# Kernel tuning notes

Measured on AMD Instinct MI355X. Metric: run time of the kernel, lower is better.

The kernel has to match this reference:

```python
import jax, jax.numpy as jnp
import numpy as np


def fps(xyz, npoint):
    # farthest point sampling, starts at index 0 (matches pointnet2 CUDA kernel)
    B, N, _ = xyz.shape
    def step(carry, _):
        min_d, last = carry
        last_xyz = jnp.take_along_axis(xyz, last[:, None, None], axis=1)  # [B,1,3]
        d = jnp.sum((xyz - last_xyz) ** 2, axis=-1)                        # [B,N]
        min_d = jnp.minimum(min_d, d)
        nxt = jnp.argmax(min_d, axis=1).astype(jnp.int32)
        return (min_d, nxt), last
    init = (jnp.full((B, N), 1e10, xyz.dtype), jnp.zeros((B,), jnp.int32))
    _, idx = jax.lax.scan(step, init, None, length=npoint)
    return jnp.transpose(idx)  # [B, npoint]


def ball_query(xyz, new_xyz, radius, nsample):
    # first nsample points within radius; pad with first hit (0 if none) -- CUDA semantics
    N = xyz.shape[1]
    d2 = jnp.sum((new_xyz[:, :, None, :] - xyz[:, None, :, :]) ** 2, axis=-1)  # [B,S,N]
    cand = jnp.where(d2 < radius * radius, jnp.arange(N, dtype=jnp.int32)[None, None, :], N)
    srt = jnp.sort(cand, axis=-1)[..., :nsample]
    first = srt[..., :1]
    first = jnp.where(first == N, 0, first)
    return jnp.where(srt == N, first, srt)  # [B,S,K]


def gather_nbrs(x, idx):
    # x [B,N,C], idx [B,S,K] -> [B,S,K,C]
    B, S, K = idx.shape
    flat = jnp.take_along_axis(x, idx.reshape(B, S * K, 1), axis=1)
    return flat.reshape(B, S, K, x.shape[-1])


def shared_mlp(x, layers):
    # 1x1 conv (+ folded eval-mode BN) + ReLU per layer
    for w, b in layers:
        x = jax.nn.relu(jnp.einsum('bskc,oc->bsko', x, w) + b)
    return x


def sa_module(xyz, feat, npoint, radius, nsample, layers):
    idx = fps(xyz, npoint)
    new_xyz = jnp.take_along_axis(xyz, idx[:, :, None], axis=1)  # [B,S,3]
    gidx = ball_query(xyz, new_xyz, radius, nsample)
    grouped = gather_nbrs(xyz, gidx) - new_xyz[:, :, None, :]    # centered local xyz
    if feat is not None:
        grouped = jnp.concatenate([grouped, gather_nbrs(feat, gidx)], axis=-1)
    x = shared_mlp(grouped, layers)
    return new_xyz, jnp.max(x, axis=2)  # max-pool over neighbors -> [B,S,Cout]


def sa_module_all(xyz, feat, layers):
    # GroupAll: concat raw (uncentered) xyz with features, one group of all points
    x = jnp.concatenate([xyz, feat], axis=-1)[:, None]  # [B,1,N,3+C]
    x = shared_mlp(x, layers)
    return jnp.max(x, axis=2)[:, 0]  # [B,Cout]


def _forward(data, ws):
    B, T, N, _ = data.shape
    xyz = data.reshape(B * T, N, 3)
    xyz, feat = sa_module(xyz, None, 256, 0.2, 32, ws[0])
    xyz, feat = sa_module(xyz, feat, 128, 0.4, 32, ws[1])
    out = sa_module_all(xyz, feat, ws[2])
    return out.reshape(B, T, -1)


DIMS = [(3, 64), (64, 64), (64, 128), (131, 128), (128, 128), (128, 256), (259, 256), (256, 512), (512, 1024)]
NAMES = ['1_0', '1_1', '1_2', '2_0', '2_1', '2_2', '3_0', '3_1', '3_2']


def setup_inputs() -> dict:
    key = jax.random.key(0)
    keys = jax.random.split(key, 1 + 2 * len(DIMS))
    inp = {'data': jax.random.normal(keys[0], (4, 8, 4096, 3), jnp.float32)}
    for i, ((cin, cout), nm) in enumerate(zip(DIMS, NAMES)):
        inp['w' + nm] = jax.random.normal(keys[1 + 2 * i], (cout, cin), jnp.float32) / np.sqrt(cin).astype(np.float32)
        inp['b' + nm] = jax.random.normal(keys[2 + 2 * i], (cout,), jnp.float32) * 0.02
    return inp


def reference(data, w1_0, b1_0, w1_1, b1_1, w1_2, b1_2,
              w2_0, b2_0, w2_1, b2_1, w2_2, b2_2,
              w3_0, b3_0, w3_1, b3_1, w3_2, b3_2):
    ws = [[(w1_0, b1_0), (w1_1, b1_1), (w1_2, b1_2)],
          [(w2_0, b2_0), (w2_1, b2_1), (w2_2, b2_2)],
          [(w3_0, b3_0), (w3_1, b3_1), (w3_2, b3_2)]]
    return _forward(data, ws)
```

## Files before the change

kernel.cpp:

```cpp
#include <hip/hip_runtime.h>
#include <hip/hip_bf16.h>
#include <cstdint>
#include <cstddef>

#define BT 32
#define N1 4096
#define S1 256
#define S2 128
#define KNB 32

typedef __attribute__((ext_vector_type(8))) short short8;
typedef __attribute__((ext_vector_type(4))) float f32x4;

__device__ __forceinline__ float sqdist(float ax, float ay, float az,
                                        float bx, float by, float bz) {
    float dx = __fsub_rn(ax, bx), dy = __fsub_rn(ay, by), dz = __fsub_rn(az, bz);
    return __fadd_rn(__fadd_rn(__fmul_rn(dx, dx), __fmul_rn(dy, dy)), __fmul_rn(dz, dz));
}

__device__ __forceinline__ unsigned short f2bf(float f) {
    unsigned u = __float_as_uint(f);
    return (unsigned short)((u + 0x7FFFu + ((u >> 16) & 1u)) >> 16);
}
__device__ __forceinline__ float bf2f(unsigned short h) {
    return __uint_as_float(((unsigned)h) << 16);
}

__device__ __forceinline__ unsigned long long packvi(float v, int idx) {
    return ((unsigned long long)__float_as_uint(v) << 32) | (unsigned)(~idx);
}

template <int CTRL>
__device__ __forceinline__ unsigned long long dppmax(unsigned long long v) {
    int lo = (int)(unsigned)(v & 0xFFFFFFFFull);
    int hi = (int)(unsigned)(v >> 32);
    int lo2 = __builtin_amdgcn_update_dpp(0, lo, CTRL, 0xF, 0xF, false);
    int hi2 = __builtin_amdgcn_update_dpp(0, hi, CTRL, 0xF, 0xF, false);
    unsigned long long o = ((unsigned long long)(unsigned)hi2 << 32) | (unsigned)lo2;
    return o > v ? o : v;
}
#define ROR1 0x121
#define ROR2 0x122
#define ROR4 0x124
#define ROR8 0x128

__global__ __launch_bounds__(256) void fps1_wconv_kernel(
    const float* __restrict__ xyz, float* __restrict__ nxz,
    const float* __restrict__ w11, const float* __restrict__ w12,
    const float* __restrict__ w20, const float* __restrict__ w21,
    const float* __restrict__ w22, const float* __restrict__ w30,
    const float* __restrict__ w31, const float* __restrict__ w32,
    unsigned short* __restrict__ wb) {
    if (blockIdx.x < 32) {
        const int b = blockIdx.x, tid = threadIdx.x;
        const int lane = tid & 63, wv = tid >> 6;
        const float* X = xyz + (size_t)b * (N1 * 3);
        __shared__ float4 s4[N1];
        __shared__ unsigned long long slots[2][16];
        __shared__ float hist[S1 * 3];
        float px[16], py[16], pz[16], md[16];
        int bidx[16];
#pragma unroll
        for (int j = 0; j < 16; ++j) {
            int i = tid + 256 * j;
            float x = X[i * 3 + 0], y = X[i * 3 + 1], z = X[i * 3 + 2];
            s4[i] = make_float4(x, y, z, 0.f);
            px[j] = x; py[j] = y; pz[j] = z;
            md[j] = 1e10f;
            bidx[j] = i;
        }
        if (tid == 0) { hist[0] = X[0]; hist[1] = X[1]; hist[2] = X[2]; }
        __syncthreads();
        float4 c0 = s4[0];
        float lx = c0.x, ly = c0.y, lz = c0.z;
        for (int t = 1; t < S1; ++t) {
            float bv = -1.0f; int bi = 0;
#pragma unroll
            for (int j = 0; j < 16; ++j) {
                float d = sqdist(px[j], py[j], pz[j], lx, ly, lz);
                float m = fminf(md[j], d);
                md[j] = m;
                if (m > bv) { bv = m; bi = bidx[j]; }
            }
            unsigned long long best = packvi(bv, bi);
            best = dppmax<ROR1>(best);
            best = dppmax<ROR2>(best);
            best = dppmax<ROR4>(best);
            best = dppmax<ROR8>(best);
            if ((lane & 15) == 0) slots[t & 1][wv * 4 + (lane >> 4)] = best;
            __syncthreads();
            unsigned long long w = slots[t & 1][lane & 15];
            w = dppmax<ROR1>(w);
            w = dppmax<ROR2>(w);
            w = dppmax<ROR4>(w);
            w = dppmax<ROR8>(w);
            int vi = (int)(~(unsigned)w);
            float4 c = s4[vi];
            lx = c.x; ly = c.y; lz = c.z;
            if (tid == 0) { hist[t * 3 + 0] = lx; hist[t * 3 + 1] = ly; hist[t * 3 + 2] = lz; }
        }
        __syncthreads();
        for (int u = tid; u < S1 * 3; u += 256) nxz[(size_t)b * S1 * 3 + u] = hist[u];
    } else {
        int u = (blockIdx.x - 32) * 256 + threadIdx.x;
        if (u >= 823296) return;
        const float* src; int base, Kp, Ko; int perm = 0;
        if      (u < 4096)   { src = w11; base = 0;      Kp = 64;  Ko = 64;  }
        else if (u < 12288)  { src = w12; base = 4096;   Kp = 64;  Ko = 64;  }
        else if (u < 36864)  { src = w20; base = 12288;  Kp = 192; Ko = 131; perm = 128; }
        else if (u < 53248)  { src = w21; base = 36864;  Kp = 128; Ko = 128; }
        else if (u < 86016)  { src = w22; base = 53248;  Kp = 128; Ko = 128; }
        else if (u < 167936) { src = w30; base = 86016;  Kp = 320; Ko = 259; perm = 256; }
        else if (u < 299008) { src = w31; base = 167936; Kp = 256; Ko = 256; }
        else                 { src = w32; base = 299008; Kp = 512; Ko = 512; }
        int local = u - base;
        int n = local / Kp, k = local - n * Kp;
        float v;
        if (perm) {
            int ksrc = (k < perm) ? (k + 3) : ((k < perm + 3) ? (k - perm) : -1);
            v = (ksrc >= 0) ? src[(size_t)n * Ko + ksrc] : 0.f;
        } else {
            v = (k < Ko) ? src[(size_t)n * Ko + k] : 0.f;
        }
        wb[u] = f2bf(v);
    }
}

__global__ __launch_bounds__(256) void ballq1_kernel(const float* __restrict__ xyz,
                                                     const float* __restrict__ nxz,
                                                     int* __restrict__ gidx) {
    const int wid = (blockIdx.x * 256 + threadIdx.x) >> 6;
    const int lane = threadIdx.x & 63;
    const int b = wid >> 8;
    const float* X = xyz + (size_t)b * (N1 * 3);
    const float* C = nxz + (size_t)wid * 3;
    const float cx = C[0], cy = C[1], cz = C[2];
    const float r2 = (float)(0.2 * 0.2);
    int* G = gidx + (size_t)wid * KNB;
    int cnt = 0, first = 0;
    bool found = false;
    for (int j0 = 0; j0 < N1 && cnt < KNB; j0 += 64) {
        int j = j0 + lane;
        float d2 = sqdist(cx, cy, cz, X[j * 3 + 0], X[j * 3 + 1], X[j * 3 + 2]);
        bool hit = d2 < r2;
        unsigned long long mask = __ballot(hit);
        if (!found && mask) { first = j0 + __builtin_ctzll(mask); found = true; }
        if (hit) {
            int pos = cnt + __popcll(mask & ((1ull << lane) - 1ull));
            if (pos < KNB) G[pos] = j;
        }
        cnt += __popcll(mask);
    }
    if (cnt < KNB) {
        int pad = found ? first : 0;
        if (lane >= cnt && lane < KNB) G[lane] = pad;
    }
}

__global__ __launch_bounds__(256) void m1_fps2_kernel(
    const float* __restrict__ xyz, const float* __restrict__ nxz,
    const int* __restrict__ g1,
    const float* __restrict__ w10, const float* __restrict__ b10,
    const unsigned short* __restrict__ w11b, const float* __restrict__ b11,
    const unsigned short* __restrict__ w12b, const float* __restrict__ b12,
    unsigned short* __restrict__ f1,
    float* __restrict__ nxz2) {
    if (blockIdx.x < 32) {
        if (threadIdx.x >= 64) return;
        const int b = blockIdx.x, lane = threadIdx.x;
        const float* X = nxz + (size_t)b * (S1 * 3);
        __shared__ float4 s4f[S1];
        float px[4], py[4], pz[4], md[4];
        int bidx[4];
#pragma unroll
        for (int j = 0; j < 4; ++j) {
            int i = lane + 64 * j;
            float x = X[i * 3 + 0], y = X[i * 3 + 1], z = X[i * 3 + 2];
            s4f[i] = make_float4(x, y, z, 0.f);
            px[j] = x; py[j] = y; pz[j] = z;
            md[j] = 1e10f;
            bidx[j] = i;
        }
        if (lane == 0) {
            nxz2[(size_t)b * S2 * 3 + 0] = X[0];
            nxz2[(size_t)b * S2 * 3 + 1] = X[1];
            nxz2[(size_t)b * S2 * 3 + 2] = X[2];
        }
        float4 cc = s4f[0];
        float lx = cc.x, ly = cc.y, lz = cc.z;
        for (int t = 1; t < S2; ++t) {
            float bv = -1.0f; int bi = 0;
#pragma unroll
            for (int j = 0; j < 4; ++j) {
                float d = sqdist(px[j], py[j], pz[j], lx, ly, lz);
                float m = fminf(md[j], d);
                md[j] = m;
                if (m > bv) { bv = m; bi = bidx[j]; }
            }
            unsigned long long best = packvi(bv, bi);
            best = dppmax<ROR1>(best);
            best = dppmax<ROR2>(best);
            best = dppmax<ROR4>(best);
            best = dppmax<ROR8>(best);
            { unsigned long long o = __shfl_xor(best, 16); best = o > best ? o : best; }
            { unsigned long long o = __shfl_xor(best, 32); best = o > best ? o : best; }
            int vi = (int)(~(unsigned)best);
            float4 c = s4f[vi];
            lx = c.x; ly = c.y; lz = c.z;
            if (lane == 0) {
                float* dst = nxz2 + ((size_t)b * S2 + t) * 3;
                dst[0] = lx; dst[1] = ly; dst[2] = lz;
            }
        }
        return;
    }
    constexpr int AP = 72;
    __shared__ __align__(16) unsigned short As[128 * AP];
    __shared__ __align__(16) unsigned short Hs[128 * AP];
    __shared__ __align__(16) unsigned short Bs[192 * AP];
    __shared__ float sxyz[128 * 3];
    const int t = threadIdx.x;
    const int lane = t & 63, w = t >> 6;
    const int r16 = lane & 15, q = lane >> 4;
    const int m0 = (blockIdx.x - 32) * 128;

    if (t < 128) {
        int row = m0 + t, bs = row >> 5, b = bs >> 8, j = g1[row];
        const float* P = xyz + ((size_t)b * N1 + j) * 3;
        const float* Cc = nxz + (size_t)bs * 3;
        sxyz[t * 3 + 0] = P[0] - Cc[0];
        sxyz[t * 3 + 1] = P[1] - Cc[1];
        sxyz[t * 3 + 2] = P[2] - Cc[2];
    }
    for (int c = t; c < 192 * 8; c += 256) {
        int row = c >> 3, ch = c & 7;
        const unsigned short* src = (row < 64) ? &w11b[row * 64 + ch * 8]
                                               : &w12b[(row - 64) * 64 + ch * 8];
        *(short8*)&Bs[row * AP + ch * 8] = *(const short8*)src;
    }
    __syncthreads();
    {
        const int r = t >> 1, half = (t & 1) * 32;
        const float x = sxyz[r * 3 + 0], y = sxyz[r * 3 + 1], z = sxyz[r * 3 + 2];
        unsigned short tmp[32];
#pragma unroll
        for (int o = 0; o < 32; ++o) {
            int oo = half + o;
            float acc = b10[oo];
            acc = fmaf(x, w10[oo * 3 + 0], acc);
            acc = fmaf(y, w10[oo * 3 + 1], acc);
            acc = fmaf(z, w10[oo * 3 + 2], acc);
            tmp[o] = f2bf(fmaxf(acc, 0.f));
        }
#pragma unroll
        for (int c2 = 0; c2 < 4; ++c2)
            *(short8*)&As[r * AP + half + c2 * 8] = *(short8*)&tmp[c2 * 8];
    }
    __syncthreads();
    {
        f32x4 acc[2][4];
#pragma unroll
        for (int i = 0; i < 2; ++i)
#pragma unroll
            for (int j = 0; j < 4; ++j) acc[i][j] = (f32x4){0.f, 0.f, 0.f, 0.f};
#pragma unroll
        for (int kk = 0; kk < 64; kk += 32) {
            short8 a0 = *(const short8*)&As[(w * 32 + r16) * AP + kk + q * 8];
            short8 a1 = *(const short8*)&As[(w * 32 + 16 + r16) * AP + kk + q * 8];
#pragma unroll
            for (int j = 0; j < 4; ++j) {
                short8 bf = *(const short8*)&Bs[(j * 16 + r16) * AP + kk + q * 8];
                acc[0][j] = __builtin_amdgcn_mfma_f32_16x16x32_bf16(a0, bf, acc[0][j], 0, 0, 0);
                acc[1][j] = __builtin_amdgcn_mfma_f32_16x16x32_bf16(a1, bf, acc[1][j], 0, 0, 0);
            }
        }
#pragma unroll
        for (int i = 0; i < 2; ++i)
#pragma unroll
            for (int j = 0; j < 4; ++j) {
                int col = j * 16 + r16;
                float bv = b11[col];
#pragma unroll
                for (int r = 0; r < 4; ++r) {
                    int row = w * 32 + i * 16 + q * 4 + r;
                    Hs[row * AP + col] = f2bf(fmaxf(acc[i][j][r] + bv, 0.f));
                }
            }
    }
    __syncthreads();
    {
        f32x4 acc[2][8];
#pragma unroll
        for (int i = 0; i < 2; ++i)
#pragma unroll
            for (int j = 0; j < 8; ++j) acc[i][j] = (f32x4){0.f, 0.f, 0.f, 0.f};
#pragma unroll
        for (int kk = 0; kk < 64; kk += 32) {
            short8 a0 = *(const short8*)&Hs[(w * 32 + r16) * AP + kk + q * 8];
            short8 a1 = *(const short8*)&Hs[(w * 32 + 16 + r16) * AP + kk + q * 8];
#pragma unroll
            for (int j = 0; j < 8; ++j) {
                short8 bf = *(const short8*)&Bs[(64 + j * 16 + r16) * AP + kk + q * 8];
                acc[0][j] = __builtin_amdgcn_mfma_f32_16x16x32_bf16(a0, bf, acc[0][j], 0, 0, 0);
                acc[1][j] = __builtin_amdgcn_mfma_f32_16x16x32_bf16(a1, bf, acc[1][j], 0, 0, 0);
            }
        }
#pragma unroll
        for (int j = 0; j < 8; ++j) {
            int col = j * 16 + r16;
            float bv = b12[col];
            float mv = 0.f;
#pragma unroll
            for (int i = 0; i < 2; ++i)
#pragma unroll
                for (int r = 0; r < 4; ++r)
                    mv = fmaxf(mv, acc[i][j][r] + bv);
            mv = fmaxf(mv, __shfl_xor(mv, 16));
            mv = fmaxf(mv, __shfl_xor(mv, 32));
            if (q == 0)
                f1[(size_t)((m0 >> 5) + w) * 128 + col] = f2bf(mv);
        }
    }
}

__global__ __launch_bounds__(256) void ballq2_kernel(const float* __restrict__ xyz1,
                                                     const float* __restrict__ nxz2,
                                                     int* __restrict__ gidx) {
    const int wid = (blockIdx.x * 256 + threadIdx.x) >> 6;
    const int lane = threadIdx.x & 63;
    const int b = wid >> 7;
    const float* X = xyz1 + (size_t)b * (S1 * 3);
    const float* C = nxz2 + (size_t)wid * 3;
    const float cx = C[0], cy = C[1], cz = C[2];
    const float r2 = (float)(0.4 * 0.4);
    int* G = gidx + (size_t)wid * KNB;
    int cnt = 0, first = 0;
    bool found = false;
    for (int j0 = 0; j0 < S1 && cnt < KNB; j0 += 64) {
        int j = j0 + lane;
        float d2 = sqdist(cx, cy, cz, X[j * 3 + 0], X[j * 3 + 1], X[j * 3 + 2]);
        bool hit = d2 < r2;
        unsigned long long mask = __ballot(hit);
        if (!found && mask) { first = j0 + __builtin_ctzll(mask); found = true; }
        if (hit) {
            int pos = cnt + __popcll(mask & ((1ull << lane) - 1ull));
            if (pos < KNB) G[pos] = j;
        }
        cnt += __popcll(mask);
    }
    if (cnt < KNB) {
        int pad = found ? first : 0;
        if (lane >= cnt && lane < KNB) G[lane] = pad;
    }
}

__global__ __launch_bounds__(256) void m2_kernel(
    const float* __restrict__ xyz1, const float* __restrict__ nxz2,
    const int* __restrict__ g2, const unsigned short* __restrict__ f1,
    const unsigned short* __restrict__ w20p, const float* __restrict__ b20,
    const unsigned short* __restrict__ w21b, const float* __restrict__ b21,
    const unsigned short* __restrict__ w22b, const float* __restrict__ b22,
    unsigned short* __restrict__ f2) {
    constexpr int AP = 72, HP = 136;
    __shared__ __align__(16) unsigned short smem[36864];
    unsigned short* R1 = smem;
    unsigned short* R2 = smem + 18432;
    unsigned short* As = R1;
    unsigned short* Bs = R1 + 9216;
    unsigned short* W21 = R1;
    unsigned short* H1 = R2;
    unsigned short* H2 = R1;
    unsigned short* Bs2 = R2;
    __shared__ int ribase[128];
    __shared__ unsigned short sxb[128 * 3];
    const int t = threadIdx.x;
    const int lane = t & 63, w = t >> 6;
    const int r16 = lane & 15, q = lane >> 4;
    const int m0 = blockIdx.x * 128;

    if (t < 128) {
        int row = m0 + t, bs = row >> 5, b = bs >> 7, j = g2[row];
        ribase[t] = (b * 256 + j) * 128;
        const float* P = xyz1 + ((size_t)b * S1 + j) * 3;
        const float* Cc = nxz2 + (size_t)bs * 3;
        sxb[t * 3 + 0] = f2bf(P[0] - Cc[0]);
        sxb[t * 3 + 1] = f2bf(P[1] - Cc[1]);
        sxb[t * 3 + 2] = f2bf(P[2] - Cc[2]);
    }
    __syncthreads();

    f32x4 acc[2][8];
#pragma unroll
    for (int i = 0; i < 2; ++i)
#pragma unroll
        for (int j = 0; j < 8; ++j) acc[i][j] = (f32x4){0.f, 0.f, 0.f, 0.f};
    for (int kt = 0; kt < 3; ++kt) {
        const int k0 = kt * 64;
        if (kt < 2) {
            for (int c = t; c < 128 * 8; c += 256) {
                int row = c >> 3, ch = c & 7;
                *(short8*)&As[row * AP + ch * 8] =
                    *(const short8*)&f1[(size_t)ribase[row] + k0 + ch * 8];
            }
        } else {
            for (int c = t; c < 128 * 8; c += 256) {
                int row = c >> 3, ch = c & 7;
                short8 v = (short8){0, 0, 0, 0, 0, 0, 0, 0};
                if (ch == 0) {
                    v[0] = (short)sxb[row * 3 + 0];
                    v[1] = (short)sxb[row * 3 + 1];
                    v[2] = (short)sxb[row * 3 + 2];
                }
                *(short8*)&As[row * AP + ch * 8] = v;
            }
        }
        for (int c = t; c < 128 * 8; c += 256) {
            int row = c >> 3, ch = c & 7;
            *(short8*)&Bs[row * AP + ch * 8] =
                *(const short8*)&w20p[(size_t)row * 192 + k0 + ch * 8];
        }
        __syncthreads();
#pragma unroll
        for (int kk = 0; kk < 64; kk += 32) {
            short8 a0 = *(const short8*)&As[(w * 32 + r16) * AP + kk + q * 8];
            short8 a1 = *(const short8*)&As[(w * 32 + 16 + r16) * AP + kk + q * 8];
#pragma unroll
            for (int j = 0; j < 8; ++j) {
                short8 bf = *(const short8*)&Bs[(j * 16 + r16) * AP + kk + q * 8];
                acc[0][j] = __builtin_amdgcn_mfma_f32_16x16x32_bf16(a0, bf, acc[0][j], 0, 0, 0);
                acc[1][j] = __builtin_amdgcn_mfma_f32_16x16x32_bf16(a1, bf, acc[1][j], 0, 0, 0);
            }
        }
        __syncthreads();
    }
#pragma unroll
    for (int i = 0; i < 2; ++i)
#pragma unroll
        for (int j = 0; j < 8; ++j) {
            int col = j * 16 + r16;
            float bv = b20[col];
#pragma unroll
            for (int r = 0; r < 4; ++r) {
                int row = w * 32 + i * 16 + q * 4 + r;
                H1[row * HP + col] = f2bf(fmaxf(acc[i][j][r] + bv, 0.f));
            }
        }
    __syncthreads();
    for (int c = t; c < 128 * 16; c += 256) {
        int row = c >> 4, ch = c & 15;
        *(short8*)&W21[row * HP + ch * 8] =
            *(const short8*)&w21b[(size_t)row * 128 + ch * 8];
    }
    __syncthreads();
#pragma unroll
    for (int i = 0; i < 2; ++i)
#pragma unroll
        for (int j = 0; j < 8; ++j) acc[i][j] = (f32x4){0.f, 0.f, 0.f, 0.f};
#pragma unroll
    for (int kk = 0; kk < 128; kk += 32) {
        short8 a0 = *(const short8*)&H1[(w * 32 + r16) * HP + kk + q * 8];
        short8 a1 = *(const short8*)&H1[(w * 32 + 16 + r16) * HP + kk + q * 8];
#pragma unroll
        for (int j = 0; j < 8; ++j) {
            short8 bf = *(const short8*)&W21[(j * 16 + r16) * HP + kk + q * 8];
            acc[0][j] = __builtin_amdgcn_mfma_f32_16x16x32_bf16(a0, bf, acc[0][j], 0, 0, 0);
            acc[1][j] = __builtin_amdgcn_mfma_f32_16x16x32_bf16(a1, bf, acc[1][j], 0, 0, 0);
        }
    }
    __syncthreads();
#pragma unroll
    for (int i = 0; i < 2; ++i)
#pragma unroll
        for (int j = 0; j < 8; ++j) {
            int col = j * 16 + r16;
            float bv = b21[col];
#pragma unroll
            for (int r = 0; r < 4; ++r) {
                int row = w * 32 + i * 16 + q * 4 + r;
                H2[row * HP + col] = f2bf(fmaxf(acc[i][j][r] + bv, 0.f));
            }
        }
    __syncthreads();

    f32x4 acc2[2][16];
#pragma unroll
    for (int i = 0; i < 2; ++i)
#pragma unroll
        for (int j = 0; j < 16; ++j) acc2[i][j] = (f32x4){0.f, 0.f, 0.f, 0.f};
    for (int kt = 0; kt < 2; ++kt) {
        const int k0 = kt * 64;
        for (int c = t; c < 256 * 8; c += 256) {
            int row = c >> 3, ch = c & 7;
            *(short8*)&Bs2[row * AP + ch * 8] =
                *(const short8*)&w22b[(size_t)row * 128 + k0 + ch * 8];
        }
        __syncthreads();
#pragma unroll
        for (int kk = 0; kk < 64; kk += 32) {
            short8 a0 = *(const short8*)&H2[(w * 32 + r16) * HP + k0 + kk + q * 8];
            short8 a1 = *(const short8*)&H2[(w * 32 + 16 + r16) * HP + k0 + kk + q * 8];
#pragma unroll
            for (int j = 0; j < 16; ++j) {
                short8 bf = *(const short8*)&Bs2[(j * 16 + r16) * AP + kk + q * 8];
                acc2[0][j] = __builtin_amdgcn_mfma_f32_16x16x32_bf16(a0, bf, acc2[0][j], 0, 0, 0);
                acc2[1][j] = __builtin_amdgcn_mfma_f32_16x16x32_bf16(a1, bf, acc2[1][j], 0, 0, 0);
            }
        }
        __syncthreads();
    }
#pragma unroll
    for (int j = 0; j < 16; ++j) {
        int col = j * 16 + r16;
        float bv = b22[col];
        float mv = 0.f;
#pragma unroll
        for (int i = 0; i < 2; ++i)
#pragma unroll
            for (int r = 0; r < 4; ++r)
                mv = fmaxf(mv, acc2[i][j][r] + bv);
        mv = fmaxf(mv, __shfl_xor(mv, 16));
        mv = fmaxf(mv, __shfl_xor(mv, 32));
        if (q == 0)
            f2[(size_t)((m0 >> 5) + w) * 256 + col] = f2bf(mv);
    }
}

__global__ __launch_bounds__(256) void l30_kernel(
    const float* __restrict__ nxz2, const unsigned short* __restrict__ f2,
    const unsigned short* __restrict__ w30p, const float* __restrict__ bias,
    unsigned short* __restrict__ C) {
    constexpr int AP = 72;
    __shared__ __align__(16) unsigned short As[128 * AP];
    __shared__ __align__(16) unsigned short Bs[128 * AP];
    const int t = threadIdx.x;
    const int lane = t & 63, w = t >> 6;
    const int r16 = lane & 15, q = lane >> 4;
    const int m0 = blockIdx.x * 128;
    const int n0 = blockIdx.y * 128;

    f32x4 acc[2][8];
#pragma unroll
    for (int i = 0; i < 2; ++i)
#pragma unroll
        for (int j = 0; j < 8; ++j) acc[i][j] = (f32x4){0.f, 0.f, 0.f, 0.f};

    for (int kt = 0; kt < 5; ++kt) {
        const int k0 = kt * 64;
        if (kt < 4) {
            for (int c = t; c < 128 * 8; c += 256) {
                int row = c >> 3, ch = c & 7;
                *(short8*)&As[row * AP + ch * 8] =
                    *(const short8*)&f2[(size_t)(m0 + row) * 256 + k0 + ch * 8];
            }
        } else {
            for (int c = t; c < 128 * 8; c += 256) {
                int row = c >> 3, ch = c & 7;
                short8 v = (short8){0, 0, 0, 0, 0, 0, 0, 0};
                if (ch == 0) {
                    const float* P = nxz2 + (size_t)(m0 + row) * 3;
                    v[0] = (short)f2bf(P[0]);
                    v[1] = (short)f2bf(P[1]);
                    v[2] = (short)f2bf(P[2]);
                }
                *(short8*)&As[row * AP + ch * 8] = v;
            }
        }
        for (int c = t; c < 128 * 8; c += 256) {
            int row = c >> 3, ch = c & 7;
            *(short8*)&Bs[row * AP + ch * 8] =
                *(const short8*)&w30p[(size_t)(n0 + row) * 320 + k0 + ch * 8];
        }
        __syncthreads();
#pragma unroll
        for (int kk = 0; kk < 64; kk += 32) {
            short8 a0 = *(const short8*)&As[(w * 32 + r16) * AP + kk + q * 8];
            short8 a1 = *(const short8*)&As[(w * 32 + 16 + r16) * AP + kk + q * 8];
#pragma unroll
            for (int j = 0; j < 8; ++j) {
                short8 bf = *(const short8*)&Bs[(j * 16 + r16) * AP + kk + q * 8];
                acc[0][j] = __builtin_amdgcn_mfma_f32_16x16x32_bf16(a0, bf, acc[0][j], 0, 0, 0);
                acc[1][j] = __builtin_amdgcn_mfma_f32_16x16x32_bf16(a1, bf, acc[1][j], 0, 0, 0);
            }
        }
        __syncthreads();
    }
#pragma unroll
    for (int i = 0; i < 2; ++i)
#pragma unroll
        for (int j = 0; j < 8; ++j) {
            int col = n0 + j * 16 + r16;
            float bv = bias[col];
#pragma unroll
            for (int r = 0; r < 4; ++r) {
                int row = m0 + w * 32 + i * 16 + q * 4 + r;
                C[(size_t)row * 256 + col] = f2bf(fmaxf(acc[i][j][r] + bv, 0.f));
            }
        }
}

template <int BM_>
__global__ __launch_bounds__(256) void mfma_gemm(const unsigned short* __restrict__ X,
                                                 const unsigned short* __restrict__ W,
                                                 const float* __restrict__ bias,
                                                 unsigned short* __restrict__ C,
                                                 int M, int N, int K) {
    constexpr int BK = 64, AP = BK + 8;
    constexpr int RW = BM_ / 64;
    constexpr int WR = BM_ / 4;
    __shared__ __align__(16) unsigned short As[BM_ * AP];
    __shared__ __align__(16) unsigned short Bs[128 * AP];
    const int t = threadIdx.x;
    const int lane = t & 63, w = t >> 6;
    const int m0 = blockIdx.x * BM_;
    const int n0 = blockIdx.y * 128;
    const int r16 = lane & 15, q = lane >> 4;

    f32x4 acc[RW][8];
#pragma unroll
    for (int i = 0; i < RW; ++i)
#pragma unroll
        for (int j = 0; j < 8; ++j) acc[i][j] = (f32x4){0.f, 0.f, 0.f, 0.f};

    for (int k0 = 0; k0 < K; k0 += BK) {
        for (int c = t; c < BM_ * 8; c += 256) {
            int row = c >> 3, ch = c & 7;
            *(short8*)&As[row * AP + ch * 8] =
                *(const short8*)&X[(size_t)(m0 + row) * K + k0 + ch * 8];
        }
        for (int c = t; c < 128 * 8; c += 256) {
            int row = c >> 3, ch = c & 7;
            *(short8*)&Bs[row * AP + ch * 8] =
                *(const short8*)&W[(size_t)(n0 + row) * K + k0 + ch * 8];
        }
        __syncthreads();
#pragma unroll
        for (int kk = 0; kk < BK; kk += 32) {
            short8 a[RW];
#pragma unroll
            for (int i = 0; i < RW; ++i)
                a[i] = *(const short8*)&As[(w * WR + i * 16 + r16) * AP + kk + q * 8];
#pragma unroll
            for (int j = 0; j < 8; ++j) {
                short8 bf = *(const short8*)&Bs[(j * 16 + r16) * AP + kk + q * 8];
#pragma unroll
                for (int i = 0; i < RW; ++i)
                    acc[i][j] = __builtin_amdgcn_mfma_f32_16x16x32_bf16(a[i], bf, acc[i][j], 0, 0, 0);
            }
        }
        __syncthreads();
    }
#pragma unroll
    for (int i = 0; i < RW; ++i)
#pragma unroll
        for (int j = 0; j < 8; ++j) {
            int col = n0 + j * 16 + r16;
            float bv = bias[col];
#pragma unroll
            for (int r = 0; r < 4; ++r) {
                int row = m0 + w * WR + i * 16 + q * 4 + r;
                C[(size_t)row * N + col] = f2bf(fmaxf(acc[i][j][r] + bv, 0.f));
            }
        }
}

__global__ __launch_bounds__(256) void gemm_pool128(const unsigned short* __restrict__ X,
                                                    const unsigned short* __restrict__ W,
                                                    const float* __restrict__ bias,
                                                    float* __restrict__ out) {
    constexpr int BK = 64, AP = BK + 8, K = 512;
    __shared__ __align__(16) unsigned short As[128 * AP];
    __shared__ __align__(16) unsigned short Bs[128 * AP];
    __shared__ float pool[4][128];
    const int t = threadIdx.x;
    const int lane = t & 63, w = t >> 6;
    const int m0 = blockIdx.x * 128;
    const int n0 = blockIdx.y * 128;
    const int r16 = lane & 15, q = lane >> 4;

    f32x4 acc[2][8];
#pragma unroll
    for (int i = 0; i < 2; ++i)
#pragma unroll
        for (int j = 0; j < 8; ++j) acc[i][j] = (f32x4){0.f, 0.f, 0.f, 0.f};

    for (int k0 = 0; k0 < K; k0 += BK) {
        for (int c = t; c < 128 * 8; c += 256) {
            int row = c >> 3, ch = c & 7;
            *(short8*)&As[row * AP + ch * 8] =
                *(const short8*)&X[(size_t)(m0 + row) * K + k0 + ch * 8];
        }
        for (int c = t; c < 128 * 8; c += 256) {
            int row = c >> 3, ch = c & 7;
            *(short8*)&Bs[row * AP + ch * 8] =
                *(const short8*)&W[(size_t)(n0 + row) * K + k0 + ch * 8];
        }
        __syncthreads();
#pragma unroll
        for (int kk = 0; kk < BK; kk += 32) {
            short8 a0 = *(const short8*)&As[(w * 32 + r16) * AP + kk + q * 8];
            short8 a1 = *(const short8*)&As[(w * 32 + 16 + r16) * AP + kk + q * 8];
#pragma unroll
            for (int j = 0; j < 8; ++j) {
                short8 bf = *(const short8*)&Bs[(j * 16 + r16) * AP + kk + q * 8];
                acc[0][j] = __builtin_amdgcn_mfma_f32_16x16x32_bf16(a0, bf, acc[0][j], 0, 0, 0);
                acc[1][j] = __builtin_amdgcn_mfma_f32_16x16x32_bf16(a1, bf, acc[1][j], 0, 0, 0);
            }
        }
        __syncthreads();
    }
#pragma unroll
    for (int j = 0; j < 8; ++j) {
        float bv = bias[n0 + j * 16 + r16];
        float mv = 0.f;
#pragma unroll
        for (int i = 0; i < 2; ++i)
#pragma unroll
            for (int r = 0; r < 4; ++r)
                mv = fmaxf(mv, acc[i][j][r] + bv);
        mv = fmaxf(mv, __shfl_xor(mv, 16));
        mv = fmaxf(mv, __shfl_xor(mv, 32));
        if (q == 0) pool[w][j * 16 + r16] = mv;
    }
    __syncthreads();
    if (t < 128) {
        float m = fmaxf(fmaxf(pool[0][t], pool[1][t]), fmaxf(pool[2][t], pool[3][t]));
        out[(size_t)blockIdx.x * 1024 + n0 + t] = m;
    }
}

extern "C" void kernel_launch(void* const* d_in, const int* in_sizes, int n_in,
                              void* d_out, int out_size, void* d_ws, size_t ws_size,
                              hipStream_t stream) {
    const float* data = (const float*)d_in[0];
    const float* w10 = (const float*)d_in[1];  const float* b10 = (const float*)d_in[2];
    const float* w11 = (const float*)d_in[3];  const float* b11 = (const float*)d_in[4];
    const float* w12 = (const float*)d_in[5];  const float* b12 = (const float*)d_in[6];
    const float* w20 = (const float*)d_in[7];  const float* b20 = (const float*)d_in[8];
    const float* w21 = (const float*)d_in[9];  const float* b21 = (const float*)d_in[10];
    const float* w22 = (const float*)d_in[11]; const float* b22 = (const float*)d_in[12];
    const float* w30 = (const float*)d_in[13]; const float* b30 = (const float*)d_in[14];
    const float* w31 = (const float*)d_in[15]; const float* b31 = (const float*)d_in[16];
    const float* w32 = (const float*)d_in[17]; const float* b32 = (const float*)d_in[18];
    float* out = (float*)d_out;

    char* ws = (char*)d_ws;
    size_t off = 0;
    auto alloc = [&](size_t bytes) -> void* {
        void* p = ws + off;
        off += (bytes + 255) & ~(size_t)255;
        return p;
    };
    float* nxz1 = (float*)alloc((size_t)BT * S1 * 3 * 4);
    int*   g1   = (int*)  alloc((size_t)BT * S1 * KNB * 4);
    float* nxz2 = (float*)alloc((size_t)BT * S2 * 3 * 4);
    int*   g2   = (int*)  alloc((size_t)BT * S2 * KNB * 4);
    unsigned short* wb  = (unsigned short*)alloc((size_t)823296 * 2);
    unsigned short* f1  = (unsigned short*)alloc((size_t)8192 * 128 * 2);
    unsigned short* f2  = (unsigned short*)alloc((size_t)4096 * 256 * 2);
    unsigned short* C1  = (unsigned short*)alloc((size_t)4096 * 256 * 2);
    unsigned short* C2  = (unsigned short*)alloc((size_t)4096 * 512 * 2);

    const unsigned short* w11b = wb + 0;
    const unsigned short* w12b = wb + 4096;
    const unsigned short* w20p = wb + 12288;
    const unsigned short* w21b = wb + 36864;
    const unsigned short* w22b = wb + 53248;
    const unsigned short* w30p = wb + 86016;
    const unsigned short* w31b = wb + 167936;
    const unsigned short* w32b = wb + 299008;

    fps1_wconv_kernel<<<32 + 3216, 256, 0, stream>>>(
        data, nxz1, w11, w12, w20, w21, w22, w30, w31, w32, wb);
    ballq1_kernel<<<(BT * S1) / 4, 256, 0, stream>>>(data, nxz1, g1);
    m1_fps2_kernel<<<32 + 2048, 256, 0, stream>>>(
        data, nxz1, g1, w10, b10, w11b, b11, w12b, b12, f1, nxz2);
    ballq2_kernel<<<(BT * S2) / 4, 256, 0, stream>>>(nxz1, nxz2, g2);
    m2_kernel<<<131072 / 128, 256, 0, stream>>>(nxz1, nxz2, g2, f1, w20p, b20, w21b, b21, w22b, b22, f2);
    l30_kernel<<<dim3(4096 / 128, 2), 256, 0, stream>>>(nxz2, f2, w30p, b30, C1);
    mfma_gemm<64><<<dim3(4096 / 64, 4), 256, 0, stream>>>(C1, w31b, b31, C2, 4096, 512, 256);
    gemm_pool128<<<dim3(4096 / 128, 8), 256, 0, stream>>>(C2, w32b, b32, out);
}
```

Measured before the change: 449.9 us.

## Fuse ball query into the MLP kernels of both set-abstraction stages

The two standalone ball-query kernels are removed. Each wave of the stage-1 and stage-2 MLP kernels now runs the neighbour search for its own centroid and keeps the 32 indices in shared memory. This drops two kernel launches and the global round-trip of the neighbour index buffers. In exchange the search latency now sits inside the MLP blocks. The stage-2 search now has to wait for the whole stage-1 kernel, which also runs the second FPS.

```diff
diff --git a/kernel.cpp b/kernel.cpp
--- a/kernel.cpp
+++ b/kernel.cpp
@@ -43,6 +43,29 @@
 #define ROR2 0x122
 #define ROR4 0x124
 #define ROR8 0x128
+
+__device__ __forceinline__ void ballq_wave(const float* __restrict__ X, int n,
+                                           float cx, float cy, float cz, float r2,
+                                           int lane, int* __restrict__ gl) {
+    int cnt = 0, first = 0;
+    bool found = false;
+    for (int j0 = 0; j0 < n && cnt < KNB; j0 += 64) {
+        int j = j0 + lane;
+        float d2 = sqdist(cx, cy, cz, X[j * 3 + 0], X[j * 3 + 1], X[j * 3 + 2]);
+        bool hit = d2 < r2;
+        unsigned long long mask = __ballot(hit);
+        if (!found && mask) { first = j0 + __builtin_ctzll(mask); found = true; }
+        if (hit) {
+            int pos = cnt + __popcll(mask & ((1ull << lane) - 1ull));
+            if (pos < KNB) gl[pos] = j;
+        }
+        cnt += __popcll(mask);
+    }
+    if (cnt < KNB) {
+        int pad = found ? first : 0;
+        if (lane >= cnt && lane < KNB) gl[lane] = pad;
+    }
+}
 
 __global__ __launch_bounds__(256) void fps1_wconv_kernel(
     const float* __restrict__ xyz, float* __restrict__ nxz,
@@ -126,40 +149,8 @@
     }
 }
 
-__global__ __launch_bounds__(256) void ballq1_kernel(const float* __restrict__ xyz,
-                                                     const float* __restrict__ nxz,
-                                                     int* __restrict__ gidx) {
-    const int wid = (blockIdx.x * 256 + threadIdx.x) >> 6;
-    const int lane = threadIdx.x & 63;
-    const int b = wid >> 8;
-    const float* X = xyz + (size_t)b * (N1 * 3);
-    const float* C = nxz + (size_t)wid * 3;
-    const float cx = C[0], cy = C[1], cz = C[2];
-    const float r2 = (float)(0.2 * 0.2);
-    int* G = gidx + (size_t)wid * KNB;
-    int cnt = 0, first = 0;
-    bool found = false;
-    for (int j0 = 0; j0 < N1 && cnt < KNB; j0 += 64) {
-        int j = j0 + lane;
-        float d2 = sqdist(cx, cy, cz, X[j * 3 + 0], X[j * 3 + 1], X[j * 3 + 2]);
-        bool hit = d2 < r2;
-        unsigned long long mask = __ballot(hit);
-        if (!found && mask) { first = j0 + __builtin_ctzll(mask); found = true; }
-        if (hit) {
-            int pos = cnt + __popcll(mask & ((1ull << lane) - 1ull));
-            if (pos < KNB) G[pos] = j;
-        }
-        cnt += __popcll(mask);
-    }
-    if (cnt < KNB) {
-        int pad = found ? first : 0;
-        if (lane >= cnt && lane < KNB) G[lane] = pad;
-    }
-}
-
-__global__ __launch_bounds__(256) void m1_fps2_kernel(
+__global__ __launch_bounds__(256) void m1bq_fps2_kernel(
     const float* __restrict__ xyz, const float* __restrict__ nxz,
-    const int* __restrict__ g1,
     const float* __restrict__ w10, const float* __restrict__ b10,
     const unsigned short* __restrict__ w11b, const float* __restrict__ b11,
     const unsigned short* __restrict__ w12b, const float* __restrict__ b12,
@@ -219,24 +210,33 @@
     __shared__ __align__(16) unsigned short Hs[128 * AP];
     __shared__ __align__(16) unsigned short Bs[192 * AP];
     __shared__ float sxyz[128 * 3];
+    __shared__ int gl[4][KNB];
     const int t = threadIdx.x;
     const int lane = t & 63, w = t >> 6;
     const int r16 = lane & 15, q = lane >> 4;
     const int m0 = (blockIdx.x - 32) * 128;
 
+    for (int c = t; c < 192 * 8; c += 256) {
+        int row = c >> 3, ch = c & 7;
+        const unsigned short* src = (row < 64) ? &w11b[row * 64 + ch * 8]
+                                               : &w12b[(row - 64) * 64 + ch * 8];
+        *(short8*)&Bs[row * AP + ch * 8] = *(const short8*)src;
+    }
+    {
+        const int cs = (m0 >> 5) + w;
+        const int bb = cs >> 8;
+        const float* Cc = nxz + (size_t)cs * 3;
+        ballq_wave(xyz + (size_t)bb * (N1 * 3), N1,
+                   Cc[0], Cc[1], Cc[2], (float)(0.2 * 0.2), lane, gl[w]);
+    }
+    __syncthreads();
     if (t < 128) {
-        int row = m0 + t, bs = row >> 5, b = bs >> 8, j = g1[row];
+        int row = m0 + t, bs = row >> 5, b = bs >> 8, j = gl[t >> 5][t & 31];
         const float* P = xyz + ((size_t)b * N1 + j) * 3;
         const float* Cc = nxz + (size_t)bs * 3;
         sxyz[t * 3 + 0] = P[0] - Cc[0];
         sxyz[t * 3 + 1] = P[1] - Cc[1];
         sxyz[t * 3 + 2] = P[2] - Cc[2];
-    }
-    for (int c = t; c < 192 * 8; c += 256) {
-        int row = c >> 3, ch = c & 7;
-        const unsigned short* src = (row < 64) ? &w11b[row * 64 + ch * 8]
-                                               : &w12b[(row - 64) * 64 + ch * 8];
-        *(short8*)&Bs[row * AP + ch * 8] = *(const short8*)src;
     }
     __syncthreads();
     {
@@ -323,40 +323,9 @@
     }
 }
 
-__global__ __launch_bounds__(256) void ballq2_kernel(const float* __restrict__ xyz1,
-                                                     const float* __restrict__ nxz2,
-                                                     int* __restrict__ gidx) {
-    const int wid = (blockIdx.x * 256 + threadIdx.x) >> 6;
-    const int lane = threadIdx.x & 63;
-    const int b = wid >> 7;
-    const float* X = xyz1 + (size_t)b * (S1 * 3);
-    const float* C = nxz2 + (size_t)wid * 3;
-    const float cx = C[0], cy = C[1], cz = C[2];
-    const float r2 = (float)(0.4 * 0.4);
-    int* G = gidx + (size_t)wid * KNB;
-    int cnt = 0, first = 0;
-    bool found = false;
-    for (int j0 = 0; j0 < S1 && cnt < KNB; j0 += 64) {
-        int j = j0 + lane;
-        float d2 = sqdist(cx, cy, cz, X[j * 3 + 0], X[j * 3 + 1], X[j * 3 + 2]);
-        bool hit = d2 < r2;
-        unsigned long long mask = __ballot(hit);
-        if (!found && mask) { first = j0 + __builtin_ctzll(mask); found = true; }
-        if (hit) {
-            int pos = cnt + __popcll(mask & ((1ull << lane) - 1ull));
-            if (pos < KNB) G[pos] = j;
-        }
-        cnt += __popcll(mask);
-    }
-    if (cnt < KNB) {
-        int pad = found ? first : 0;
-        if (lane >= cnt && lane < KNB) G[lane] = pad;
-    }
-}
-
-__global__ __launch_bounds__(256) void m2_kernel(
+__global__ __launch_bounds__(256) void m2bq_kernel(
     const float* __restrict__ xyz1, const float* __restrict__ nxz2,
-    const int* __restrict__ g2, const unsigned short* __restrict__ f1,
+    const unsigned short* __restrict__ f1,
     const unsigned short* __restrict__ w20p, const float* __restrict__ b20,
     const unsigned short* __restrict__ w21b, const float* __restrict__ b21,
     const unsigned short* __restrict__ w22b, const float* __restrict__ b22,
@@ -373,13 +342,22 @@
     unsigned short* Bs2 = R2;
     __shared__ int ribase[128];
     __shared__ unsigned short sxb[128 * 3];
+    __shared__ int gl2[4][KNB];
     const int t = threadIdx.x;
     const int lane = t & 63, w = t >> 6;
     const int r16 = lane & 15, q = lane >> 4;
     const int m0 = blockIdx.x * 128;
 
+    {
+        const int cs = (m0 >> 5) + w;
+        const int bb = cs >> 7;
+        const float* Cc = nxz2 + (size_t)cs * 3;
+        ballq_wave(xyz1 + (size_t)bb * (S1 * 3), S1,
+                   Cc[0], Cc[1], Cc[2], (float)(0.4 * 0.4), lane, gl2[w]);
+    }
+    __syncthreads();
     if (t < 128) {
-        int row = m0 + t, bs = row >> 5, b = bs >> 7, j = g2[row];
+        int row = m0 + t, bs = row >> 5, b = bs >> 7, j = gl2[t >> 5][t & 31];
         ribase[t] = (b * 256 + j) * 128;
         const float* P = xyz1 + ((size_t)b * S1 + j) * 3;
         const float* Cc = nxz2 + (size_t)bs * 3;
@@ -751,9 +729,7 @@
         return p;
     };
     float* nxz1 = (float*)alloc((size_t)BT * S1 * 3 * 4);
-    int*   g1   = (int*)  alloc((size_t)BT * S1 * KNB * 4);
     float* nxz2 = (float*)alloc((size_t)BT * S2 * 3 * 4);
-    int*   g2   = (int*)  alloc((size_t)BT * S2 * KNB * 4);
     unsigned short* wb  = (unsigned short*)alloc((size_t)823296 * 2);
     unsigned short* f1  = (unsigned short*)alloc((size_t)8192 * 128 * 2);
     unsigned short* f2  = (unsigned short*)alloc((size_t)4096 * 256 * 2);
@@ -771,11 +747,10 @@
 
     fps1_wconv_kernel<<<32 + 3216, 256, 0, stream>>>(
         data, nxz1, w11, w12, w20, w21, w22, w30, w31, w32, wb);
-    ballq1_kernel<<<(BT * S1) / 4, 256, 0, stream>>>(data, nxz1, g1);
-    m1_fps2_kernel<<<32 + 2048, 256, 0, stream>>>(
-        data, nxz1, g1, w10, b10, w11b, b11, w12b, b12, f1, nxz2);
-    ballq2_kernel<<<(BT * S2) / 4, 256, 0, stream>>>(nxz1, nxz2, g2);
-    m2_kernel<<<131072 / 128, 256, 0, stream>>>(nxz1, nxz2, g2, f1, w20p, b20, w21b, b21, w22b, b22, f2);
+    m1bq_fps2_kernel<<<32 + 2048, 256, 0, stream>>>(
+        data, nxz1, w10, b10, w11b, b11, w12b, b12, f1, nxz2);
+    m2bq_kernel<<<131072 / 128, 256, 0, stream>>>(
+        nxz1, nxz2, f1, w20p, b20, w21b, b21, w22b, b22, f2);
     l30_kernel<<<dim3(4096 / 128, 2), 256, 0, stream>>>(nxz2, f2, w30p, b30, C1);
     mfma_gemm<64><<<dim3(4096 / 64, 4), 256, 0, stream>>>(C1, w31b, b31, C2, 4096, 512, 256);
     gemm_pool128<<<dim3(4096 / 128, 8), 256, 0, stream>>>(C2, w32b, b32, out);
```

After: 505.6 us. 12.4% more time.
